# Performance work log

Measured on AMD Instinct MI355X. Metric: run time of the kernel, lower is better.

The kernel has to match this reference:

```python
import jax, jax.numpy as jnp
import numpy as np

K = 3
STRIDE = 1
PAD = 1


def _conv2d(x, w, b):
    y = jax.lax.conv_general_dilated(
        x, w, window_strides=(STRIDE, STRIDE),
        padding=[(PAD, PAD), (PAD, PAD)],
        dimension_numbers=("NCHW", "OIHW", "NCHW"))
    return y + b[None, :, None, None]


def _bilinear_sample(xb, py, px):
    # xb: [C, H, W]; py, px: [K2, Ho, Wo] float sample coords
    C, H, W = xb.shape
    y0 = jnp.floor(py)
    x0 = jnp.floor(px)
    ay = py - y0  # frac weights
    ax = px - x0
    out = jnp.zeros((C,) + py.shape, dtype=xb.dtype)
    corners = [
        (y0, x0, (1.0 - ay) * (1.0 - ax)),
        (y0, x0 + 1.0, (1.0 - ay) * ax),
        (y0 + 1.0, x0, ay * (1.0 - ax)),
        (y0 + 1.0, x0 + 1.0, ay * ax),
    ]
    for yc, xc, wgt in corners:
        valid = (yc >= 0) & (yc < H) & (xc >= 0) & (xc < W)
        yi = jnp.clip(yc, 0, H - 1).astype(jnp.int32)
        xi = jnp.clip(xc, 0, W - 1).astype(jnp.int32)
        g = xb[:, yi, xi]  # [C, K2, Ho, Wo]
        out = out + g * (wgt * valid.astype(xb.dtype))[None]
    return out


def _deform_forward(x, weight, bias, p_weight, p_bias):
    B, Cin, H, W = x.shape
    Cout = weight.shape[0]
    K2 = K * K
    # offset / mask prediction conv
    pout = _conv2d(x, p_weight, p_bias)  # [B, 3*K2, Ho, Wo]
    o1, o2, m = jnp.split(pout, 3, axis=1)
    offset = jnp.concatenate([o1, o2], axis=1)  # [B, 2*K2, Ho, Wo]
    mask = jax.nn.sigmoid(m)  # [B, K2, Ho, Wo]
    Ho, Wo = mask.shape[2], mask.shape[3]
    # torchvision layout: channel 2k = dy_k, 2k+1 = dx_k
    off = offset.reshape(B, K2, 2, Ho, Wo)
    dy, dx = off[:, :, 0], off[:, :, 1]  # [B, K2, Ho, Wo]
    ki = (jnp.arange(K2) // K).astype(x.dtype)  # kernel row
    kj = (jnp.arange(K2) % K).astype(x.dtype)   # kernel col
    base_y = jnp.arange(Ho, dtype=x.dtype) * STRIDE - PAD  # [Ho]
    base_x = jnp.arange(Wo, dtype=x.dtype) * STRIDE - PAD  # [Wo]
    py = base_y[None, None, :, None] + ki[None, :, None, None] + dy
    px = base_x[None, None, None, :] + kj[None, :, None, None] + dx
    sampled = jax.vmap(_bilinear_sample)(x, py, px)  # [B, Cin, K2, Ho, Wo]
    sampled = sampled * mask[:, None]
    w = weight.reshape(Cout, Cin, K2)
    out = jnp.einsum('bckhw,ock->bohw', sampled, w) + bias[None, :, None, None]
    return out


def setup_inputs() -> dict:
    key = jax.random.key(0)
    k1, k2, k3 = jax.random.split(key, 3)
    B, Cin, Cout, H, W = 4, 256, 256, 64, 64
    x = jax.random.normal(k1, (B, Cin, H, W), dtype=jnp.float32)
    fan_in = Cin * K * K
    weight = jax.random.normal(k2, (Cout, Cin, K, K), dtype=jnp.float32) / np.sqrt(fan_in)
    bias = jnp.zeros((Cout,), dtype=jnp.float32)
    # small random offset/mask predictor (zero-init in the original; randomized
    # here so the deformable sampling path is exercised)
    p_weight = jax.random.normal(k3, (3 * K * K, Cin, K, K), dtype=jnp.float32) * 0.02
    p_bias = jnp.zeros((3 * K * K,), dtype=jnp.float32)
    return {"x": x, "weight": weight, "bias": bias, "p_weight": p_weight, "p_bias": p_bias}


def reference(x, weight, bias, p_weight, p_bias):
    return _deform_forward(x, weight, bias, p_weight, p_bias)
```

## Files before the change

kernel.cpp:

```cpp
#include <hip/hip_runtime.h>
#include <stdint.h>


#define CIN 256
#define COUT 256
#define HWS 4096
#define MTOT 16384
#define KTOT 2304
#define SPLITK 8

typedef __attribute__((ext_vector_type(8))) short bf16x8;
typedef __attribute__((ext_vector_type(4))) float f32x4;

__device__ __forceinline__ unsigned short f2bf(float f) {
  unsigned int u = __float_as_uint(f);
  unsigned int r = (u + 0x7fffu + ((u >> 16) & 1u)) >> 16;
  return (unsigned short)r;
}
__device__ __forceinline__ float bf2f(unsigned short u) {
  return __uint_as_float(((unsigned int)u) << 16);
}
__device__ __forceinline__ float bflo(unsigned int u) { return __uint_as_float(u << 16); }
__device__ __forceinline__ float bfhi(unsigned int u) { return __uint_as_float(u & 0xffff0000u); }

__device__ __forceinline__ void gload_lds16(const void* g, void* l) {
  __builtin_amdgcn_global_load_lds((const __attribute__((address_space(1))) void*)g,
                                   (__attribute__((address_space(3))) void*)l, 16, 0, 0);
}

#define GLOAD8(D, P)  asm volatile("global_load_dwordx2 %0, %1, off" : "=v"(D) : "v"(P))
#define GLOAD16(D, P) asm volatile("global_load_dwordx4 %0, %1, off" : "=v"(D) : "v"(P))
#define WAITVM(N)                                            \
  {                                                          \
    asm volatile("s_waitcnt vmcnt(" #N ")" ::: "memory");    \
    __builtin_amdgcn_sched_barrier(0);                       \
  }
#define BARRIER_LGKM                                                  \
  { asm volatile("s_waitcnt lgkmcnt(0)\n\ts_barrier" ::: "memory"); }

#define ASW(c, rr) ((c) ^ (((rr) & 7) << 3))

__global__ __launch_bounds__(256) void prep_and_transpose(const float* __restrict__ x,
                                                          const float* __restrict__ w,
                                                          const float* __restrict__ pw,
                                                          unsigned short* __restrict__ xt,
                                                          unsigned short* __restrict__ WB,
                                                          unsigned short* __restrict__ PWs,
                                                          unsigned short* __restrict__ zerop) {
  __shared__ float tile[32][33];
  int bid = blockIdx.x;
  if (bid < 4096) {
    int b = bid >> 10;
    int rest = bid & 1023;
    int hw0 = (rest & 127) * 32;
    int c0 = ((rest >> 7) & 7) * 32;
    int tx = threadIdx.x & 31, ty = threadIdx.x >> 5;
    for (int i = ty; i < 32; i += 8)
      tile[i][tx] = x[(size_t)(b * CIN + c0 + i) * HWS + hw0 + tx];
    __syncthreads();
    for (int r = ty; r < 32; r += 8)
      xt[(size_t)(b * HWS + hw0 + r) * CIN + c0 + tx] = f2bf(tile[tx][r]);
  } else {
    int idx = (bid - 4096) * 256 + threadIdx.x;
    if (idx < 512)
      *(uint4*)(zerop + idx * 8) = make_uint4(0, 0, 0, 0);
    if (idx < KTOT * COUT) {
      int f = idx;
      int e = f & 7;
      int row = (f >> 3) & 15;
      int quad = (f >> 7) & 3;
      int j = (f >> 9) & 15;
      int t = f >> 13;
      int kk = t * 32 + quad * 8 + e;
      int o = j * 16 + row;
      int k = kk >> 8, c = kk & 255;
      WB[f] = f2bf(w[o * KTOT + c * 9 + k]);
    } else {
      int f2 = idx - KTOT * COUT;
      int t_ = f2 & 7;
      int rest = f2 >> 3;
      int j = rest & 31;
      int kk = (rest >> 5) * 8 + t_;
      int k = kk >> 8, c = kk & 255;
      float v = (j < 27) ? pw[j * KTOT + c * 9 + k] : 0.0f;
      PWs[f2] = f2bf(v);
    }
  }
}

__global__ __launch_bounds__(256) void offset_conv_sk(const unsigned short* __restrict__ xt,
                                                      const unsigned short* __restrict__ PWs,
                                                      const unsigned short* __restrict__ zerop,
                                                      float* __restrict__ Pbuf) {
  __shared__ unsigned short Al[64 * 32];
  __shared__ unsigned short Bl[1024];
  int tid = threadIdx.x;
  int lane = tid & 63, wv = tid >> 6;
  int mt = (blockIdx.x & 7) * 32 + (blockIdx.x >> 3);
  int m0 = mt * 64;
  int s = blockIdx.y;
  int b = m0 >> 12;
  int hw0 = m0 & 4095;
  f32x4 acc[2] = {};

  for (int tt = 0; tt < 72 / SPLITK; ++tt) {
    int t = s * (72 / SPLITK) + tt;
    int k = t >> 3, c0 = (t & 7) * 32;
    int dyk = k / 3 - 1;
    int dxk = k % 3 - 1;
    __syncthreads();
    if (tid < 128)
      gload_lds16(PWs + (size_t)t * 1024 + tid * 8, &Bl[tid * 8]);
    {
      int r = tid >> 2;
      int hw = hw0 + r;
      int h = hw >> 6, wwp = hw & 63;
      int y = h + dyk, xx = wwp + dxk;
      bool valid = ((unsigned)y < 64u) && ((unsigned)xx < 64u);
      const unsigned short* src = valid
          ? xt + ((size_t)((b << 12) + (y << 6) + xx) << 8) + c0 + (tid & 3) * 8
          : zerop;
      gload_lds16(src, &Al[tid * 8]);
    }
    __syncthreads();
    int row = lane & 15, quad = lane >> 4;
    bf16x8 af = *(const bf16x8*)&Al[(wv * 16 + row) * 32 + quad * 8];
    for (int j = 0; j < 2; ++j) {
      bf16x8 bfr = *(const bf16x8*)&Bl[(quad * 32 + j * 16 + row) * 8];
      acc[j] = __builtin_amdgcn_mfma_f32_16x16x32_bf16(af, bfr, acc[j], 0, 0, 0);
    }
  }

  int row = lane & 15, quad = lane >> 4;
  for (int j = 0; j < 2; ++j) {
    int n = j * 16 + row;
    for (int r_ = 0; r_ < 4; ++r_) {
      int m = m0 + wv * 16 + quad * 4 + r_;
      Pbuf[((size_t)s * MTOT + m) * 32 + n] = acc[j][r_];
    }
  }
}

__global__ __launch_bounds__(256) void index_prep(const float* __restrict__ Pbuf,
                                                  const float* __restrict__ p_bias,
                                                  int4* __restrict__ DIW) {
  int gid = blockIdx.x * 256 + threadIdx.x;
  int m = gid / 9;
  int k = gid - m * 9;

  float dy = p_bias[2 * k];
  float dx = p_bias[2 * k + 1];
  float mv = p_bias[18 + k];
#pragma unroll
  for (int s = 0; s < SPLITK; ++s) {
    const float* p = Pbuf + ((size_t)s * MTOT + m) * 32;
    dy += p[2 * k];
    dx += p[2 * k + 1];
    mv += p[18 + k];
  }
  float mk = 1.0f / (1.0f + __expf(-mv));

  int hw = m & 4095, h = hw >> 6, ww = hw & 63;
  float py = (float)(h - 1 + k / 3) + dy;
  float px = (float)(ww - 1 + k % 3) + dx;
  float y0f = floorf(py), x0f = floorf(px);
  float ay = py - y0f, ax = px - x0f;
  int y0 = (int)y0f, x0 = (int)x0f;

  float w00 = (1.f - ay) * (1.f - ax) * mk;
  float w01 = (1.f - ay) * ax * mk;
  float w10 = ay * (1.f - ax) * mk;
  float w11 = ay * ax * mk;

  float vy0 = ((unsigned)y0 < 64u) ? 1.f : 0.f;
  float vy1 = ((unsigned)(y0 + 1) < 64u) ? 1.f : 0.f;
  float vx0 = ((unsigned)x0 < 64u) ? 1.f : 0.f;
  float vx1 = ((unsigned)(x0 + 1) < 64u) ? 1.f : 0.f;
  w00 *= vy0 * vx0; w01 *= vy0 * vx1; w10 *= vy1 * vx0; w11 *= vy1 * vx1;

  int yc0 = min(max(y0, 0), 63), yc1 = min(max(y0 + 1, 0), 63);
  int xc0 = min(max(x0, 0), 63), xc1 = min(max(x0 + 1, 0), 63);

  DIW[(size_t)gid * 2] = make_int4((yc0 * 64 + xc0) * 256, (yc0 * 64 + xc1) * 256,
                                   (yc1 * 64 + xc0) * 256, (yc1 * 64 + xc1) * 256);
  float4 w4 = make_float4(w00, w01, w10, w11);
  ((float4*)DIW)[(size_t)gid * 2 + 1] = w4;
}

__device__ __forceinline__ void bilin4p(const uint2 c00, const uint2 c01,
                                        const uint2 c10, const uint2 c11,
                                        const float4 w4, unsigned short* dst) {
  float v0 = w4.x * bflo(c00.x) + w4.y * bflo(c01.x) + w4.z * bflo(c10.x) + w4.w * bflo(c11.x);
  float v1 = w4.x * bfhi(c00.x) + w4.y * bfhi(c01.x) + w4.z * bfhi(c10.x) + w4.w * bfhi(c11.x);
  float v2 = w4.x * bflo(c00.y) + w4.y * bflo(c01.y) + w4.z * bflo(c10.y) + w4.w * bflo(c11.y);
  float v3 = w4.x * bfhi(c00.y) + w4.y * bfhi(c01.y) + w4.z * bfhi(c10.y) + w4.w * bfhi(c11.y);
  ushort4 o;
  o.x = f2bf(v0); o.y = f2bf(v1); o.z = f2bf(v2); o.w = f2bf(v3);
  *(ushort4*)dst = o;
}

#define MFMA16P                                                                          \
  acc[0][0] = __builtin_amdgcn_mfma_f32_16x16x32_bf16(afr0, bB0, acc[0][0], 0, 0, 0);    \
  acc[0][1] = __builtin_amdgcn_mfma_f32_16x16x32_bf16(afr0, bB1, acc[0][1], 0, 0, 0);    \
  acc[1][0] = __builtin_amdgcn_mfma_f32_16x16x32_bf16(afr1, bB0, acc[1][0], 0, 0, 0);    \
  acc[1][1] = __builtin_amdgcn_mfma_f32_16x16x32_bf16(afr1, bB1, acc[1][1], 0, 0, 0);    \
  acc[2][0] = __builtin_amdgcn_mfma_f32_16x16x32_bf16(afr2, bB0, acc[2][0], 0, 0, 0);    \
  acc[2][1] = __builtin_amdgcn_mfma_f32_16x16x32_bf16(afr2, bB1, acc[2][1], 0, 0, 0);    \
  acc[3][0] = __builtin_amdgcn_mfma_f32_16x16x32_bf16(afr3, bB0, acc[3][0], 0, 0, 0);    \
  acc[3][1] = __builtin_amdgcn_mfma_f32_16x16x32_bf16(afr3, bB1, acc[3][1], 0, 0, 0);    \
  acc[0][0] = __builtin_amdgcn_mfma_f32_16x16x32_bf16(afr4, bB2, acc[0][0], 0, 0, 0);    \
  acc[0][1] = __builtin_amdgcn_mfma_f32_16x16x32_bf16(afr4, bB3, acc[0][1], 0, 0, 0);    \
  acc[1][0] = __builtin_amdgcn_mfma_f32_16x16x32_bf16(afr5, bB2, acc[1][0], 0, 0, 0);    \
  acc[1][1] = __builtin_amdgcn_mfma_f32_16x16x32_bf16(afr5, bB3, acc[1][1], 0, 0, 0);    \
  acc[2][0] = __builtin_amdgcn_mfma_f32_16x16x32_bf16(afr6, bB2, acc[2][0], 0, 0, 0);    \
  acc[2][1] = __builtin_amdgcn_mfma_f32_16x16x32_bf16(afr6, bB3, acc[2][1], 0, 0, 0);    \
  acc[3][0] = __builtin_amdgcn_mfma_f32_16x16x32_bf16(afr7, bB2, acc[3][0], 0, 0, 0);    \
  acc[3][1] = __builtin_amdgcn_mfma_f32_16x16x32_bf16(afr7, bB3, acc[3][1], 0, 0, 0);

#define FITER_P(P, PAR, GI0, GI1, GI2, GI3, GI4, GI5, GI6, GI7,                          \
                GC0, GC1, GC2, GC3, GC4, GC5, GC6, GC7)                                  \
  {                                                                                      \
    const unsigned short* bt0 = bpb + (size_t)(2 * (P)) * 8192;                          \
    GLOAD16(bB0, bt0);                                                                   \
    GLOAD16(bB1, bt0 + 512);                                                             \
    GLOAD16(bB2, bt0 + 8192);                                                            \
    GLOAD16(bB3, bt0 + 8192 + 512);                                                      \
    if ((((P) + 2) & 3) == 0) dI4 = Tbl[r][((P) + 2) >> 2][0];                           \
    int cb = ((2 * (P) + 4) & 7) * 32 + qo;                                              \
    GLOAD8(GI0, xtb + dI4.x + cb);                                                       \
    GLOAD8(GI1, xtb + dI4.y + cb);                                                       \
    GLOAD8(GI2, xtb + dI4.z + cb);                                                       \
    GLOAD8(GI3, xtb + dI4.w + cb);                                                       \
    GLOAD8(GI4, xtb + dI4.x + cb + 32);                                                  \
    GLOAD8(GI5, xtb + dI4.y + cb + 32);                                                  \
    GLOAD8(GI6, xtb + dI4.z + cb + 32);                                                  \
    GLOAD8(GI7, xtb + dI4.w + cb + 32);                                                  \
    afr0 = *(const bf16x8*)&As[PAR][row][ASW(quad * 8, row)];                            \
    afr1 = *(const bf16x8*)&As[PAR][16 + row][ASW(quad * 8, row)];                       \
    afr2 = *(const bf16x8*)&As[PAR][32 + row][ASW(quad * 8, row)];                       \
    afr3 = *(const bf16x8*)&As[PAR][48 + row][ASW(quad * 8, row)];                       \
    afr4 = *(const bf16x8*)&As[PAR][row][ASW(32 + quad * 8, row)];                       \
    afr5 = *(const bf16x8*)&As[PAR][16 + row][ASW(32 + quad * 8, row)];                  \
    afr6 = *(const bf16x8*)&As[PAR][32 + row][ASW(32 + quad * 8, row)];                  \
    afr7 = *(const bf16x8*)&As[PAR][48 + row][ASW(32 + quad * 8, row)];                  \
    if ((((P) + 1) & 3) == 0) dW4 = *(float4*)&Tbl[r][((P) + 1) >> 2][1];                \
    WAITVM(12)                                                                           \
    bilin4p(GC0, GC1, GC2, GC3, dW4, &As[PAR ^ 1][r][ASW(qo, r)]);                       \
    bilin4p(GC4, GC5, GC6, GC7, dW4, &As[PAR ^ 1][r][ASW(32 + qo, r)]);                  \
    WAITVM(8)                                                                            \
    MFMA16P                                                                              \
    BARRIER_LGKM                                                                         \
  }

__global__ __launch_bounds__(512, 2) void fused_gemm(const unsigned short* __restrict__ xt,
                                                     const int4* __restrict__ DIW,
                                                     const unsigned short* __restrict__ WB,
                                                     const float* __restrict__ bias,
                                                     float* __restrict__ out) {
  __shared__ unsigned short As[2][64][64];
  __shared__ int4 Tbl[64][9][2];

  int tid = threadIdx.x;
  int lane = tid & 63, wv = tid >> 6;
  int mt = (blockIdx.x & 7) * 32 + (blockIdx.x >> 3);
  int mb = mt * 64;
  int b = mb >> 12;
  int hw0 = mb & 4095;
  const unsigned short* xtb = xt + ((size_t)b << 20);

  {
    const int4* src = DIW + (size_t)mb * 18;
    int4* dst = (int4*)Tbl;
    for (int i = tid; i < 1152; i += 512)
      gload_lds16(src + i, dst + i);
  }
  __syncthreads();

  int r = tid >> 3;
  int qo = (tid & 7) * 4;

  int4 dI4 = Tbl[r][0][0];
  float4 dW4 = *(float4*)&Tbl[r][0][1];

  int row = lane & 15, quad = lane >> 4;
  const unsigned short* bpb = WB + (size_t)(wv * 2) * 512 + quad * 128 + row * 8;

  f32x4 acc[4][2] = {};
  uint2 gA0, gA1, gA2, gA3, gA4, gA5, gA6, gA7;
  uint2 gB0, gB1, gB2, gB3, gB4, gB5, gB6, gB7;
  bf16x8 bB0, bB1, bB2, bB3;
  bf16x8 afr0, afr1, afr2, afr3, afr4, afr5, afr6, afr7;

  {
    uint2 p00 = *(const uint2*)(xtb + dI4.x + qo);
    uint2 p01 = *(const uint2*)(xtb + dI4.y + qo);
    uint2 p10 = *(const uint2*)(xtb + dI4.z + qo);
    uint2 p11 = *(const uint2*)(xtb + dI4.w + qo);
    bilin4p(p00, p01, p10, p11, dW4, &As[0][r][ASW(qo, r)]);
    p00 = *(const uint2*)(xtb + dI4.x + 32 + qo);
    p01 = *(const uint2*)(xtb + dI4.y + 32 + qo);
    p10 = *(const uint2*)(xtb + dI4.z + 32 + qo);
    p11 = *(const uint2*)(xtb + dI4.w + 32 + qo);
    bilin4p(p00, p01, p10, p11, dW4, &As[0][r][ASW(32 + qo, r)]);
    GLOAD8(gB0, xtb + dI4.x + 64 + qo);
    GLOAD8(gB1, xtb + dI4.y + 64 + qo);
    GLOAD8(gB2, xtb + dI4.z + 64 + qo);
    GLOAD8(gB3, xtb + dI4.w + 64 + qo);
    GLOAD8(gB4, xtb + dI4.x + 96 + qo);
    GLOAD8(gB5, xtb + dI4.y + 96 + qo);
    GLOAD8(gB6, xtb + dI4.z + 96 + qo);
    GLOAD8(gB7, xtb + dI4.w + 96 + qo);
  }
  BARRIER_LGKM

#pragma unroll 1
  for (int p = 0; p < 34; p += 2) {
    FITER_P(p,     0, gA0, gA1, gA2, gA3, gA4, gA5, gA6, gA7,
                      gB0, gB1, gB2, gB3, gB4, gB5, gB6, gB7)
    FITER_P(p + 1, 1, gB0, gB1, gB2, gB3, gB4, gB5, gB6, gB7,
                      gA0, gA1, gA2, gA3, gA4, gA5, gA6, gA7)
  }

  {
    const unsigned short* bt0 = bpb + (size_t)68 * 8192;
    GLOAD16(bB0, bt0);
    GLOAD16(bB1, bt0 + 512);
    GLOAD16(bB2, bt0 + 8192);
    GLOAD16(bB3, bt0 + 8192 + 512);
    afr0 = *(const bf16x8*)&As[0][row][ASW(quad * 8, row)];
    afr1 = *(const bf16x8*)&As[0][16 + row][ASW(quad * 8, row)];
    afr2 = *(const bf16x8*)&As[0][32 + row][ASW(quad * 8, row)];
    afr3 = *(const bf16x8*)&As[0][48 + row][ASW(quad * 8, row)];
    afr4 = *(const bf16x8*)&As[0][row][ASW(32 + quad * 8, row)];
    afr5 = *(const bf16x8*)&As[0][16 + row][ASW(32 + quad * 8, row)];
    afr6 = *(const bf16x8*)&As[0][32 + row][ASW(32 + quad * 8, row)];
    afr7 = *(const bf16x8*)&As[0][48 + row][ASW(32 + quad * 8, row)];
    WAITVM(4)
    bilin4p(gB0, gB1, gB2, gB3, dW4, &As[1][r][ASW(qo, r)]);
    bilin4p(gB4, gB5, gB6, gB7, dW4, &As[1][r][ASW(32 + qo, r)]);
    WAITVM(0)
    MFMA16P
    BARRIER_LGKM
  }
  {
    const unsigned short* bt0 = bpb + (size_t)70 * 8192;
    GLOAD16(bB0, bt0);
    GLOAD16(bB1, bt0 + 512);
    GLOAD16(bB2, bt0 + 8192);
    GLOAD16(bB3, bt0 + 8192 + 512);
    afr0 = *(const bf16x8*)&As[1][row][ASW(quad * 8, row)];
    afr1 = *(const bf16x8*)&As[1][16 + row][ASW(quad * 8, row)];
    afr2 = *(const bf16x8*)&As[1][32 + row][ASW(quad * 8, row)];
    afr3 = *(const bf16x8*)&As[1][48 + row][ASW(quad * 8, row)];
    afr4 = *(const bf16x8*)&As[1][row][ASW(32 + quad * 8, row)];
    afr5 = *(const bf16x8*)&As[1][16 + row][ASW(32 + quad * 8, row)];
    afr6 = *(const bf16x8*)&As[1][32 + row][ASW(32 + quad * 8, row)];
    afr7 = *(const bf16x8*)&As[1][48 + row][ASW(32 + quad * 8, row)];
    WAITVM(0)
    MFMA16P
  }

#pragma unroll
  for (int j = 0; j < 2; ++j) {
    int o = wv * 32 + j * 16 + row;
    float bo = bias[o];
#pragma unroll
    for (int i = 0; i < 4; ++i) {
      int hw = hw0 + i * 16 + quad * 4;
      float4 v;
      v.x = acc[i][j][0] + bo;
      v.y = acc[i][j][1] + bo;
      v.z = acc[i][j][2] + bo;
      v.w = acc[i][j][3] + bo;
      *(float4*)(out + (((size_t)(b * COUT + o)) << 12) + hw) = v;
    }
  }
}

extern "C" void kernel_launch(void* const* d_in, const int* in_sizes, int n_in,
                              void* d_out, int out_size, void* d_ws, size_t ws_size,
                              hipStream_t stream) {
  const float* x        = (const float*)d_in[0];
  const float* weight   = (const float*)d_in[1];
  const float* bias     = (const float*)d_in[2];
  const float* p_weight = (const float*)d_in[3];
  const float* p_bias   = (const float*)d_in[4];
  float* out = (float*)d_out;
  char* ws = (char*)d_ws;

  const size_t OFF_XT   = 0;
  const size_t OFF_WB   = OFF_XT + 8388608;
  const size_t OFF_PW   = OFF_WB + 1179648;
  const size_t OFF_P    = OFF_PW + 147456;
  const size_t OFF_ZP   = OFF_P + 16777216;
  const size_t OFF_DIW  = OFF_ZP + 8192;

  unsigned short* xt    = (unsigned short*)(ws + OFF_XT);
  unsigned short* WB    = (unsigned short*)(ws + OFF_WB);
  unsigned short* PWs   = (unsigned short*)(ws + OFF_PW);
  float* Pbuf           = (float*)(ws + OFF_P);
  unsigned short* zerop = (unsigned short*)(ws + OFF_ZP);
  int4* DIW             = (int4*)(ws + OFF_DIW);

  prep_and_transpose<<<4096 + 2592, 256, 0, stream>>>(x, weight, p_weight, xt, WB, PWs, zerop);
  offset_conv_sk<<<dim3(MTOT / 64, SPLITK), 256, 0, stream>>>(xt, PWs, zerop, Pbuf);
  index_prep<<<576, 256, 0, stream>>>(Pbuf, p_bias, DIW);
  fused_gemm<<<256, 512, 0, stream>>>(xt, DIW, WB, bias, out);
}
```

Before: 137.1 us.

## Widen gather loads to 16 bytes and prefetch weight tiles one step ahead

The gather of bilinear corner values moves from two 8-byte loads per corner to one 16-byte load, so each thread produces 8 bf16 outputs per step. The weight (B) fragments are now double-buffered and loaded one iteration ahead, which lets the MFMAs run before the bilinear interpolation instead of after it. The aim is fewer memory instructions and better overlap between matrix math and the gather/interpolation work. In exchange the kernel holds more live registers and the waitcnt accounting becomes more delicate.

```diff
diff --git a/kernel.cpp b/kernel.cpp
--- a/kernel.cpp
+++ b/kernel.cpp
@@ -28,7 +28,6 @@
                                    (__attribute__((address_space(3))) void*)l, 16, 0, 0);
 }
 
-#define GLOAD8(D, P)  asm volatile("global_load_dwordx2 %0, %1, off" : "=v"(D) : "v"(P))
 #define GLOAD16(D, P) asm volatile("global_load_dwordx4 %0, %1, off" : "=v"(D) : "v"(P))
 #define WAITVM(N)                                            \
   {                                                          \
@@ -187,54 +186,58 @@
   ((float4*)DIW)[(size_t)gid * 2 + 1] = w4;
 }
 
-__device__ __forceinline__ void bilin4p(const uint2 c00, const uint2 c01,
-                                        const uint2 c10, const uint2 c11,
+__device__ __forceinline__ void bilin8p(const uint4 c00, const uint4 c01,
+                                        const uint4 c10, const uint4 c11,
                                         const float4 w4, unsigned short* dst) {
-  float v0 = w4.x * bflo(c00.x) + w4.y * bflo(c01.x) + w4.z * bflo(c10.x) + w4.w * bflo(c11.x);
-  float v1 = w4.x * bfhi(c00.x) + w4.y * bfhi(c01.x) + w4.z * bfhi(c10.x) + w4.w * bfhi(c11.x);
-  float v2 = w4.x * bflo(c00.y) + w4.y * bflo(c01.y) + w4.z * bflo(c10.y) + w4.w * bflo(c11.y);
-  float v3 = w4.x * bfhi(c00.y) + w4.y * bfhi(c01.y) + w4.z * bfhi(c10.y) + w4.w * bfhi(c11.y);
-  ushort4 o;
-  o.x = f2bf(v0); o.y = f2bf(v1); o.z = f2bf(v2); o.w = f2bf(v3);
-  *(ushort4*)dst = o;
-}
-
-#define MFMA16P                                                                          \
-  acc[0][0] = __builtin_amdgcn_mfma_f32_16x16x32_bf16(afr0, bB0, acc[0][0], 0, 0, 0);    \
-  acc[0][1] = __builtin_amdgcn_mfma_f32_16x16x32_bf16(afr0, bB1, acc[0][1], 0, 0, 0);    \
-  acc[1][0] = __builtin_amdgcn_mfma_f32_16x16x32_bf16(afr1, bB0, acc[1][0], 0, 0, 0);    \
-  acc[1][1] = __builtin_amdgcn_mfma_f32_16x16x32_bf16(afr1, bB1, acc[1][1], 0, 0, 0);    \
-  acc[2][0] = __builtin_amdgcn_mfma_f32_16x16x32_bf16(afr2, bB0, acc[2][0], 0, 0, 0);    \
-  acc[2][1] = __builtin_amdgcn_mfma_f32_16x16x32_bf16(afr2, bB1, acc[2][1], 0, 0, 0);    \
-  acc[3][0] = __builtin_amdgcn_mfma_f32_16x16x32_bf16(afr3, bB0, acc[3][0], 0, 0, 0);    \
-  acc[3][1] = __builtin_amdgcn_mfma_f32_16x16x32_bf16(afr3, bB1, acc[3][1], 0, 0, 0);    \
-  acc[0][0] = __builtin_amdgcn_mfma_f32_16x16x32_bf16(afr4, bB2, acc[0][0], 0, 0, 0);    \
-  acc[0][1] = __builtin_amdgcn_mfma_f32_16x16x32_bf16(afr4, bB3, acc[0][1], 0, 0, 0);    \
-  acc[1][0] = __builtin_amdgcn_mfma_f32_16x16x32_bf16(afr5, bB2, acc[1][0], 0, 0, 0);    \
-  acc[1][1] = __builtin_amdgcn_mfma_f32_16x16x32_bf16(afr5, bB3, acc[1][1], 0, 0, 0);    \
-  acc[2][0] = __builtin_amdgcn_mfma_f32_16x16x32_bf16(afr6, bB2, acc[2][0], 0, 0, 0);    \
-  acc[2][1] = __builtin_amdgcn_mfma_f32_16x16x32_bf16(afr6, bB3, acc[2][1], 0, 0, 0);    \
-  acc[3][0] = __builtin_amdgcn_mfma_f32_16x16x32_bf16(afr7, bB2, acc[3][0], 0, 0, 0);    \
-  acc[3][1] = __builtin_amdgcn_mfma_f32_16x16x32_bf16(afr7, bB3, acc[3][1], 0, 0, 0);
-
-#define FITER_P(P, PAR, GI0, GI1, GI2, GI3, GI4, GI5, GI6, GI7,                          \
-                GC0, GC1, GC2, GC3, GC4, GC5, GC6, GC7)                                  \
+  uint4 o;
+  float v0, v1;
+  v0 = w4.x * bflo(c00.x) + w4.y * bflo(c01.x) + w4.z * bflo(c10.x) + w4.w * bflo(c11.x);
+  v1 = w4.x * bfhi(c00.x) + w4.y * bfhi(c01.x) + w4.z * bfhi(c10.x) + w4.w * bfhi(c11.x);
+  o.x = (unsigned)f2bf(v0) | ((unsigned)f2bf(v1) << 16);
+  v0 = w4.x * bflo(c00.y) + w4.y * bflo(c01.y) + w4.z * bflo(c10.y) + w4.w * bflo(c11.y);
+  v1 = w4.x * bfhi(c00.y) + w4.y * bfhi(c01.y) + w4.z * bfhi(c10.y) + w4.w * bfhi(c11.y);
+  o.y = (unsigned)f2bf(v0) | ((unsigned)f2bf(v1) << 16);
+  v0 = w4.x * bflo(c00.z) + w4.y * bflo(c01.z) + w4.z * bflo(c10.z) + w4.w * bflo(c11.z);
+  v1 = w4.x * bfhi(c00.z) + w4.y * bfhi(c01.z) + w4.z * bfhi(c10.z) + w4.w * bfhi(c11.z);
+  o.z = (unsigned)f2bf(v0) | ((unsigned)f2bf(v1) << 16);
+  v0 = w4.x * bflo(c00.w) + w4.y * bflo(c01.w) + w4.z * bflo(c10.w) + w4.w * bflo(c11.w);
+  v1 = w4.x * bfhi(c00.w) + w4.y * bfhi(c01.w) + w4.z * bfhi(c10.w) + w4.w * bfhi(c11.w);
+  o.w = (unsigned)f2bf(v0) | ((unsigned)f2bf(v1) << 16);
+  *(uint4*)dst = o;
+}
+
+#define MFMA16P(B0, B1, B2, B3)                                                          \
+  acc[0][0] = __builtin_amdgcn_mfma_f32_16x16x32_bf16(afr0, B0, acc[0][0], 0, 0, 0);     \
+  acc[0][1] = __builtin_amdgcn_mfma_f32_16x16x32_bf16(afr0, B1, acc[0][1], 0, 0, 0);     \
+  acc[1][0] = __builtin_amdgcn_mfma_f32_16x16x32_bf16(afr1, B0, acc[1][0], 0, 0, 0);     \
+  acc[1][1] = __builtin_amdgcn_mfma_f32_16x16x32_bf16(afr1, B1, acc[1][1], 0, 0, 0);     \
+  acc[2][0] = __builtin_amdgcn_mfma_f32_16x16x32_bf16(afr2, B0, acc[2][0], 0, 0, 0);     \
+  acc[2][1] = __builtin_amdgcn_mfma_f32_16x16x32_bf16(afr2, B1, acc[2][1], 0, 0, 0);     \
+  acc[3][0] = __builtin_amdgcn_mfma_f32_16x16x32_bf16(afr3, B0, acc[3][0], 0, 0, 0);     \
+  acc[3][1] = __builtin_amdgcn_mfma_f32_16x16x32_bf16(afr3, B1, acc[3][1], 0, 0, 0);     \
+  acc[0][0] = __builtin_amdgcn_mfma_f32_16x16x32_bf16(afr4, B2, acc[0][0], 0, 0, 0);     \
+  acc[0][1] = __builtin_amdgcn_mfma_f32_16x16x32_bf16(afr4, B3, acc[0][1], 0, 0, 0);     \
+  acc[1][0] = __builtin_amdgcn_mfma_f32_16x16x32_bf16(afr5, B2, acc[1][0], 0, 0, 0);     \
+  acc[1][1] = __builtin_amdgcn_mfma_f32_16x16x32_bf16(afr5, B3, acc[1][1], 0, 0, 0);     \
+  acc[2][0] = __builtin_amdgcn_mfma_f32_16x16x32_bf16(afr6, B2, acc[2][0], 0, 0, 0);     \
+  acc[2][1] = __builtin_amdgcn_mfma_f32_16x16x32_bf16(afr6, B3, acc[2][1], 0, 0, 0);     \
+  acc[3][0] = __builtin_amdgcn_mfma_f32_16x16x32_bf16(afr7, B2, acc[3][0], 0, 0, 0);     \
+  acc[3][1] = __builtin_amdgcn_mfma_f32_16x16x32_bf16(afr7, B3, acc[3][1], 0, 0, 0);
+
+#define FITER_P2(P, PAR, GI0, GI1, GI2, GI3, GC0, GC1, GC2, GC3,                         \
+                 BC0, BC1, BC2, BC3, BI0, BI1, BI2, BI3)                                 \
   {                                                                                      \
-    const unsigned short* bt0 = bpb + (size_t)(2 * (P)) * 8192;                          \
-    GLOAD16(bB0, bt0);                                                                   \
-    GLOAD16(bB1, bt0 + 512);                                                             \
-    GLOAD16(bB2, bt0 + 8192);                                                            \
-    GLOAD16(bB3, bt0 + 8192 + 512);                                                      \
+    const unsigned short* btn = bpb + (size_t)(2 * ((P) + 1)) * 8192;                    \
+    GLOAD16(BI0, btn);                                                                   \
+    GLOAD16(BI1, btn + 512);                                                             \
+    GLOAD16(BI2, btn + 8192);                                                            \
+    GLOAD16(BI3, btn + 8192 + 512);                                                      \
     if ((((P) + 2) & 3) == 0) dI4 = Tbl[r][((P) + 2) >> 2][0];                           \
-    int cb = ((2 * (P) + 4) & 7) * 32 + qo;                                              \
-    GLOAD8(GI0, xtb + dI4.x + cb);                                                       \
-    GLOAD8(GI1, xtb + dI4.y + cb);                                                       \
-    GLOAD8(GI2, xtb + dI4.z + cb);                                                       \
-    GLOAD8(GI3, xtb + dI4.w + cb);                                                       \
-    GLOAD8(GI4, xtb + dI4.x + cb + 32);                                                  \
-    GLOAD8(GI5, xtb + dI4.y + cb + 32);                                                  \
-    GLOAD8(GI6, xtb + dI4.z + cb + 32);                                                  \
-    GLOAD8(GI7, xtb + dI4.w + cb + 32);                                                  \
+    int cb = ((2 * (P) + 4) & 7) * 32 + qo8;                                             \
+    GLOAD16(GI0, xtb + dI4.x + cb);                                                      \
+    GLOAD16(GI1, xtb + dI4.y + cb);                                                      \
+    GLOAD16(GI2, xtb + dI4.z + cb);                                                      \
+    GLOAD16(GI3, xtb + dI4.w + cb);                                                      \
     afr0 = *(const bf16x8*)&As[PAR][row][ASW(quad * 8, row)];                            \
     afr1 = *(const bf16x8*)&As[PAR][16 + row][ASW(quad * 8, row)];                       \
     afr2 = *(const bf16x8*)&As[PAR][32 + row][ASW(quad * 8, row)];                       \
@@ -245,10 +248,9 @@
     afr7 = *(const bf16x8*)&As[PAR][48 + row][ASW(32 + quad * 8, row)];                  \
     if ((((P) + 1) & 3) == 0) dW4 = *(float4*)&Tbl[r][((P) + 1) >> 2][1];                \
     WAITVM(12)                                                                           \
-    bilin4p(GC0, GC1, GC2, GC3, dW4, &As[PAR ^ 1][r][ASW(qo, r)]);                       \
-    bilin4p(GC4, GC5, GC6, GC7, dW4, &As[PAR ^ 1][r][ASW(32 + qo, r)]);                  \
+    MFMA16P(BC0, BC1, BC2, BC3)                                                          \
     WAITVM(8)                                                                            \
-    MFMA16P                                                                              \
+    bilin8p(GC0, GC1, GC2, GC3, dW4, &As[PAR ^ 1][r][ASW(qo8, r)]);                      \
     BARRIER_LGKM                                                                         \
   }
 
@@ -277,7 +279,7 @@
   __syncthreads();
 
   int r = tid >> 3;
-  int qo = (tid & 7) * 4;
+  int qo8 = (tid & 7) * 8;
 
   int4 dI4 = Tbl[r][0][0];
   float4 dW4 = *(float4*)&Tbl[r][0][1];
@@ -286,47 +288,44 @@
   const unsigned short* bpb = WB + (size_t)(wv * 2) * 512 + quad * 128 + row * 8;
 
   f32x4 acc[4][2] = {};
-  uint2 gA0, gA1, gA2, gA3, gA4, gA5, gA6, gA7;
-  uint2 gB0, gB1, gB2, gB3, gB4, gB5, gB6, gB7;
+  uint4 gA0, gA1, gA2, gA3;
+  uint4 gB0, gB1, gB2, gB3;
+  bf16x8 bA0, bA1, bA2, bA3;
   bf16x8 bB0, bB1, bB2, bB3;
   bf16x8 afr0, afr1, afr2, afr3, afr4, afr5, afr6, afr7;
 
   {
-    uint2 p00 = *(const uint2*)(xtb + dI4.x + qo);
-    uint2 p01 = *(const uint2*)(xtb + dI4.y + qo);
-    uint2 p10 = *(const uint2*)(xtb + dI4.z + qo);
-    uint2 p11 = *(const uint2*)(xtb + dI4.w + qo);
-    bilin4p(p00, p01, p10, p11, dW4, &As[0][r][ASW(qo, r)]);
-    p00 = *(const uint2*)(xtb + dI4.x + 32 + qo);
-    p01 = *(const uint2*)(xtb + dI4.y + 32 + qo);
-    p10 = *(const uint2*)(xtb + dI4.z + 32 + qo);
-    p11 = *(const uint2*)(xtb + dI4.w + 32 + qo);
-    bilin4p(p00, p01, p10, p11, dW4, &As[0][r][ASW(32 + qo, r)]);
-    GLOAD8(gB0, xtb + dI4.x + 64 + qo);
-    GLOAD8(gB1, xtb + dI4.y + 64 + qo);
-    GLOAD8(gB2, xtb + dI4.z + 64 + qo);
-    GLOAD8(gB3, xtb + dI4.w + 64 + qo);
-    GLOAD8(gB4, xtb + dI4.x + 96 + qo);
-    GLOAD8(gB5, xtb + dI4.y + 96 + qo);
-    GLOAD8(gB6, xtb + dI4.z + 96 + qo);
-    GLOAD8(gB7, xtb + dI4.w + 96 + qo);
+    uint4 p00 = *(const uint4*)(xtb + dI4.x + qo8);
+    uint4 p01 = *(const uint4*)(xtb + dI4.y + qo8);
+    uint4 p10 = *(const uint4*)(xtb + dI4.z + qo8);
+    uint4 p11 = *(const uint4*)(xtb + dI4.w + qo8);
+    bilin8p(p00, p01, p10, p11, dW4, &As[0][r][ASW(qo8, r)]);
+    GLOAD16(bA0, bpb);
+    GLOAD16(bA1, bpb + 512);
+    GLOAD16(bA2, bpb + 8192);
+    GLOAD16(bA3, bpb + 8192 + 512);
+    int cb1 = 64 + qo8;
+    GLOAD16(gA0, xtb + dI4.x + cb1);
+    GLOAD16(gA1, xtb + dI4.y + cb1);
+    GLOAD16(gA2, xtb + dI4.z + cb1);
+    GLOAD16(gA3, xtb + dI4.w + cb1);
   }
   BARRIER_LGKM
 
 #pragma unroll 1
   for (int p = 0; p < 34; p += 2) {
-    FITER_P(p,     0, gA0, gA1, gA2, gA3, gA4, gA5, gA6, gA7,
-                      gB0, gB1, gB2, gB3, gB4, gB5, gB6, gB7)
-    FITER_P(p + 1, 1, gB0, gB1, gB2, gB3, gB4, gB5, gB6, gB7,
-                      gA0, gA1, gA2, gA3, gA4, gA5, gA6, gA7)
+    FITER_P2(p,     0, gB0, gB1, gB2, gB3, gA0, gA1, gA2, gA3,
+                       bA0, bA1, bA2, bA3, bB0, bB1, bB2, bB3)
+    FITER_P2(p + 1, 1, gA0, gA1, gA2, gA3, gB0, gB1, gB2, gB3,
+                       bB0, bB1, bB2, bB3, bA0, bA1, bA2, bA3)
   }
 
   {
-    const unsigned short* bt0 = bpb + (size_t)68 * 8192;
-    GLOAD16(bB0, bt0);
-    GLOAD16(bB1, bt0 + 512);
-    GLOAD16(bB2, bt0 + 8192);
-    GLOAD16(bB3, bt0 + 8192 + 512);
+    const unsigned short* btn = bpb + (size_t)70 * 8192;
+    GLOAD16(bB0, btn);
+    GLOAD16(bB1, btn + 512);
+    GLOAD16(bB2, btn + 8192);
+    GLOAD16(bB3, btn + 8192 + 512);
     afr0 = *(const bf16x8*)&As[0][row][ASW(quad * 8, row)];
     afr1 = *(const bf16x8*)&As[0][16 + row][ASW(quad * 8, row)];
     afr2 = *(const bf16x8*)&As[0][32 + row][ASW(quad * 8, row)];
@@ -335,19 +334,13 @@
     afr5 = *(const bf16x8*)&As[0][16 + row][ASW(32 + quad * 8, row)];
     afr6 = *(const bf16x8*)&As[0][32 + row][ASW(32 + quad * 8, row)];
     afr7 = *(const bf16x8*)&As[0][48 + row][ASW(32 + quad * 8, row)];
+    WAITVM(8)
+    MFMA16P(bA0, bA1, bA2, bA3)
     WAITVM(4)
-    bilin4p(gB0, gB1, gB2, gB3, dW4, &As[1][r][ASW(qo, r)]);
-    bilin4p(gB4, gB5, gB6, gB7, dW4, &As[1][r][ASW(32 + qo, r)]);
-    WAITVM(0)
-    MFMA16P
+    bilin8p(gA0, gA1, gA2, gA3, dW4, &As[1][r][ASW(qo8, r)]);
     BARRIER_LGKM
   }
   {
-    const unsigned short* bt0 = bpb + (size_t)70 * 8192;
-    GLOAD16(bB0, bt0);
-    GLOAD16(bB1, bt0 + 512);
-    GLOAD16(bB2, bt0 + 8192);
-    GLOAD16(bB3, bt0 + 8192 + 512);
     afr0 = *(const bf16x8*)&As[1][row][ASW(quad * 8, row)];
     afr1 = *(const bf16x8*)&As[1][16 + row][ASW(quad * 8, row)];
     afr2 = *(const bf16x8*)&As[1][32 + row][ASW(quad * 8, row)];
@@ -357,7 +350,7 @@
     afr6 = *(const bf16x8*)&As[1][32 + row][ASW(32 + quad * 8, row)];
     afr7 = *(const bf16x8*)&As[1][48 + row][ASW(32 + quad * 8, row)];
     WAITVM(0)
-    MFMA16P
+    MFMA16P(bB0, bB1, bB2, bB3)
   }
 
 #pragma unroll
```

New measurement: 130.8 us. 1.05x faster.
